# Performance work log

Measured on AMD Instinct MI355X. Metric: run time of the kernel, lower is better.

Reference implementation:

```python
import jax, jax.numpy as jnp
import numpy as np

B, P, H, W = 8, 128, 32, 32
NC = 4                 # num_classes = NUM_REL_GROUP + 1
DOBJ = 4424            # 2*DOBJ = 8848
CIN = 256
C = 128 + 8848         # 8976 GCN channel dim


def setup_inputs() -> dict:
    key = jax.random.key(0)
    ks = jax.random.split(key, 24)
    s = 0.02  # weight scale to keep activations moderate
    inp = {
        "x": jax.random.normal(ks[0], (B, CIN, H, W), jnp.float32),
        "rel_pair_idxs": jax.random.randint(ks[1], (B, P, 2), 0, 640, dtype=jnp.int32),
        "obj_rep": jax.random.normal(ks[2], (640, DOBJ), jnp.float32),
        # ADD_GCN params
        "fc_w": jax.random.normal(ks[3], (NC, CIN), jnp.float32) * s,
        "ct_w": jax.random.normal(ks[4], (128, CIN), jnp.float32) * s,
        "ct_b": jnp.zeros((128,), jnp.float32),
        # DynamicGraphConvolution params
        "A": jax.random.normal(ks[5], (NC, NC), jnp.float32) * 0.25,          # static_adj conv1d (no bias)
        "sw_w": jax.random.normal(ks[6], (C, C), jnp.float32) * s / np.sqrt(C) * 30,
        "sw_b": jnp.zeros((C,), jnp.float32),
        "cg_w": jax.random.normal(ks[7], (C, C), jnp.float32) * s / np.sqrt(C) * 30,
        "cg_b": jnp.zeros((C,), jnp.float32),
        "bn_g": jnp.ones((C,), jnp.float32),
        "bn_b": jnp.zeros((C,), jnp.float32),
        "bn_m": jnp.zeros((C,), jnp.float32),
        "bn_v": jnp.ones((C,), jnp.float32),
        "co_w": jax.random.normal(ks[8], (NC, 2 * C), jnp.float32) * s / np.sqrt(C) * 30,
        "co_b": jnp.zeros((NC,), jnp.float32),
        "dw_w": jax.random.normal(ks[9], (C, C), jnp.float32) * s / np.sqrt(C) * 30,
        "dw_b": jnp.zeros((C,), jnp.float32),
        "ll_w": jax.random.normal(ks[10], (NC, C), jnp.float32) * s / np.sqrt(C) * 30,
        "ll_b": jnp.zeros((NC,), jnp.float32),
        "mask_mat": jnp.eye(NC, dtype=jnp.float32),
    }
    return inp


def reference(x, rel_pair_idxs, obj_rep, fc_w, ct_w, ct_b, A, sw_w, sw_b,
              cg_w, cg_b, bn_g, bn_b, bn_m, bn_v, co_w, co_b, dw_w, dw_b,
              ll_w, ll_b, mask_mat):
    leaky = lambda t: jax.nn.leaky_relu(t, 0.2)
    b, cin, h, w = x.shape
    xr = x.reshape(b, cin, h * w)                                  # (B,256,HW)

    # forward_classification_sm: fc -> topk(1).mean == max over spatial
    y = jnp.einsum('oc,bcs->bos', fc_w, xr)                        # (B,NC,HW)
    out1 = y.max(-1)                                               # (B,NC)

    # forward_sam
    mask = jax.nn.sigmoid(y)                                       # (B,NC,HW)
    v = jnp.einsum('oc,bcs->bos', ct_w, xr) + ct_b[None, :, None]  # (B,128,HW)
    v = jnp.einsum('bcs,bns->bcn', v, mask)                        # (B,128,NC)

    # pairwise object features (gather), tiled over NC node slots
    o1 = obj_rep[rel_pair_idxs[..., 0]]                            # (B,P,DOBJ)
    o2 = obj_rep[rel_pair_idxs[..., 1]]
    pf = jnp.concatenate([o1, o2], -1)                             # (B,P,8848)
    p = pf.shape[1]
    pf = jnp.broadcast_to(pf[..., None], pf.shape + (NC,))         # (B,P,8848,NC)
    vb = jnp.broadcast_to(v[:, None], (b, p) + v.shape[1:])        # (B,P,128,NC)
    g = jnp.concatenate([pf, vb], 2).reshape(b * p, C, NC)         # (BP,C,NC)

    # --- DynamicGraphConvolution ---
    # static GCN: node-mix conv1d (no bias) + leaky, then channel 1x1 conv + leaky
    xs = leaky(jnp.einsum('nm,pcm->pcn', A, g))                    # (BP,C,NC)
    xs = leaky(jnp.einsum('oc,pcn->pon', sw_w, xs) + sw_b[None, :, None])
    hg = g + xs

    # dynamic adjacency
    glb = hg.mean(-1)                                              # (BP,C) gap
    glb = glb @ cg_w.T + cg_b                                      # conv_global (1x1)
    glb = (glb - bn_m) * jax.lax.rsqrt(bn_v + 1e-5) * bn_g + bn_b  # BN (eval)
    glb = leaky(glb)
    # conv_create_co_mat over cat([glb_expand, hg], ch) without materializing cat
    adj = jax.nn.sigmoid(
        jnp.einsum('oc,pc->po', co_w[:, :C], glb)[:, :, None]
        + jnp.einsum('oc,pcn->pon', co_w[:, C:], hg)
        + co_b[None, :, None])                                     # (BP,NC,NC)

    # dynamic GCN
    hd = leaky(jnp.einsum('pcn,pnm->pcm', hg, adj))
    z = leaky(jnp.einsum('oc,pcn->pon', dw_w, hd) + dw_b[None, :, None])  # (BP,C,NC)

    # head: last_linear + leaky, masked diagonal sum
    out2 = leaky(jnp.einsum('oc,pcn->pon', ll_w, z) + ll_b[None, :, None])  # (BP,NC,NC)
    out2 = (out2 * jax.lax.stop_gradient(mask_mat)).sum(-1)        # (BP,NC)

    o1b = jnp.broadcast_to(out1[:, None], (b, p, NC)).reshape(b * p, NC)
    return ((o1b + out2) * 0.5).reshape(b, p, NC)
```

## Files before the change

kernel.cpp:

```cpp
#include <hip/hip_runtime.h>
#include <stdint.h>

#define DEVI __device__ __forceinline__

typedef unsigned short u16;
typedef __bf16 bf16x8 __attribute__((ext_vector_type(8)));
typedef float f32x4 __attribute__((ext_vector_type(4)));
typedef u16 u16x8 __attribute__((ext_vector_type(8)));

DEVI u16 f2bf(float f){
  union { float f; unsigned u; } v; v.f = f;
  unsigned r = v.u + 0x7FFFu + ((v.u >> 16) & 1u);
  return (u16)(r >> 16);
}
DEVI float bf2f(u16 h){
  union { unsigned u; float f; } v; v.u = ((unsigned)h) << 16;
  return v.f;
}
DEVI float lky(float t){ return t > 0.f ? t : 0.2f * t; }

#define GLD16(gp, lp) __builtin_amdgcn_global_load_lds( \
    (const __attribute__((address_space(1))) void*)(gp), \
    (__attribute__((address_space(3))) void*)(lp), 16, 0, 0)


DEVI void stage_half(const u16* __restrict__ G, size_t grow0, int kcol, int Kp,
                     u16* lds, int t)
{
  #pragma unroll
  for (int j = 0; j < 2; ++j){
    const int off16 = j*512 + t;
    const int rl = off16 >> 3, sl = off16 & 7;
    const u16* gp = G + (grow0 + rl)*(size_t)Kp + kcol + ((sl ^ (rl & 7))*8);
    GLD16(gp, lds + off16*8);
  }
}

template<int RB, int RA>
DEVI void ph_reads(const u16* __restrict__ Ab, const u16* __restrict__ Bb,
                   bf16x8 (&afr)[4][2], bf16x8 (&bfr)[4][2],
                   int wr, int wc, int l4, int l15)
{
  if constexpr (RA >= 0){
    #pragma unroll
    for (int m = 0; m < 4; ++m){
      const int r = wr*128 + RA*64 + m*16 + l15;
      afr[m][0] = *(const bf16x8*)&Ab[r*64 + (((0+l4) ^ (r & 7))*8)];
      afr[m][1] = *(const bf16x8*)&Ab[r*64 + (((4+l4) ^ (r & 7))*8)];
    }
  }
  if constexpr (RB >= 0){
    #pragma unroll
    for (int nn = 0; nn < 2; ++nn){
      const int r = wc*64 + (RB+nn)*16 + l15;
      bfr[RB+nn][0] = *(const bf16x8*)&Bb[r*64 + (((0+l4) ^ (r & 7))*8)];
      bfr[RB+nn][1] = *(const bf16x8*)&Bb[r*64 + (((4+l4) ^ (r & 7))*8)];
    }
  }
}

template<int MH, int NH, int VM>
DEVI void ph_mfma(bf16x8 (&afr)[4][2], bf16x8 (&bfr)[4][2], f32x4 (&acc)[8][4])
{
  __builtin_amdgcn_s_barrier();
  __builtin_amdgcn_s_setprio(1);
  #pragma unroll
  for (int m = 0; m < 4; ++m)
    #pragma unroll
    for (int nn = 0; nn < 2; ++nn)
      #pragma unroll
      for (int ks = 0; ks < 2; ++ks)
        acc[MH*4+m][NH+nn] = __builtin_amdgcn_mfma_f32_16x16x32_bf16(
            afr[m][ks], bfr[NH+nn][ks], acc[MH*4+m][NH+nn], 0, 0, 0);
  __builtin_amdgcn_s_setprio(0);
  if constexpr (VM == 4){
    asm volatile("s_waitcnt vmcnt(4)" ::: "memory");
  }
  __builtin_amdgcn_s_barrier();
}

template<int EPI>
__global__ __launch_bounds__(512, 2)
void gemm256(const u16* __restrict__ A, const u16* __restrict__ B,
             int Kp, int Nt, int SN, int Mreal, float* __restrict__ C, long long ldc,
             const float* __restrict__ bias, const float* __restrict__ scale,
             const float* __restrict__ off, const float* __restrict__ llw,
             float* __restrict__ oacc,
             int ngemm, const float* __restrict__ cvt_src, int cvt_srows,
             int cvt_scols, int cvt_lstride, u16* __restrict__ cvt_dst,
             int cvt_kp, int cvt_prows, int cvt_nblk)
{
  __shared__ __align__(16) u16 As[2][16384];
  __shared__ __align__(16) u16 Bs[2][16384];

  if ((int)blockIdx.x >= ngemm){
    const int bid = blockIdx.x - ngemm;
    const int nch = cvt_kp >> 3;
    for (int r = bid; r < cvt_prows; r += cvt_nblk){
      for (int ch = threadIdx.x; ch < nch; ch += 512){
        const int k = ch*8;
        u16 o[8];
        if (r < cvt_srows){
          #pragma unroll
          for (int i=0;i<8;i++){
            const int kk = k + i;
            o[i] = (kk < cvt_scols) ? f2bf(cvt_src[(size_t)r*cvt_lstride + kk]) : (u16)0;
          }
        } else {
          #pragma unroll
          for (int i=0;i<8;i++) o[i] = 0;
        }
        u16x8 vv = { o[0],o[1],o[2],o[3],o[4],o[5],o[6],o[7] };
        *(u16x8*)&cvt_dst[(size_t)r*cvt_kp + k] = vv;
      }
    }
    return;
  }

  const int t    = threadIdx.x;
  const int lane = t & 63;
  const int wid  = t >> 6;
  const int wr = wid >> 2, wc = wid & 3;
  const int l4 = lane >> 4, l15 = lane & 15;

  const int nwg = ngemm;
  const int xc = blockIdx.x & 7, pp = blockIdx.x >> 3;
  const int qq = nwg >> 3, rr = nwg & 7;
  const int wg = (xc < rr ? xc*(qq+1) : rr*(qq+1) + (xc-rr)*qq) + pp;
  const int strip_sz = (nwg / Nt) * SN;
  const int strip = wg / strip_sz, srem = wg % strip_sz;
  const int mt = srem / SN, nt = strip*SN + srem % SN;

  const size_t am0 = (size_t)mt*256;
  const size_t bn0 = (size_t)nt*256;

  f32x4 acc[8][4];
  #pragma unroll
  for (int i = 0; i < 8; ++i)
    #pragma unroll
    for (int j = 0; j < 4; ++j) acc[i][j] = f32x4{0.f,0.f,0.f,0.f};
  bf16x8 afr[4][2], bfr[4][2];

  const int NT2 = Kp >> 6;
  const int NI  = NT2 >> 1;

  stage_half(A, am0+0,   0,  Kp, &As[0][0],    t);
  stage_half(A, am0+128, 0,  Kp, &As[0][8192], t);
  stage_half(B, bn0+0,   0,  Kp, &Bs[0][0],    t);
  stage_half(B, bn0+128, 0,  Kp, &Bs[0][8192], t);
  stage_half(B, bn0+0,   64, Kp, &Bs[1][0],    t);
  stage_half(B, bn0+128, 64, Kp, &Bs[1][8192], t);
  asm volatile("s_waitcnt vmcnt(4)" ::: "memory");
  __builtin_amdgcn_s_barrier();

  for (int i = 0; i < NI; ++i){
    const int k1  = 2*i + 1;
    const int ts0 = (2*i+2 < NT2) ? 2*i+2 : 2*i;
    const int ts1 = (2*i+3 < NT2) ? 2*i+3 : 2*i+1;
    ph_reads<0,0>(&As[0][0], &Bs[0][0], afr, bfr, wr, wc, l4, l15);
    stage_half(A, am0+0,   k1*64,  Kp, &As[1][0],    t);
    ph_mfma<0,0,-1>(afr, bfr, acc);
    ph_reads<2,-1>(&As[0][0], &Bs[0][0], afr, bfr, wr, wc, l4, l15);
    stage_half(A, am0+128, k1*64,  Kp, &As[1][8192], t);
    ph_mfma<0,2,-1>(afr, bfr, acc);
    ph_reads<-1,1>(&As[0][0], &Bs[0][0], afr, bfr, wr, wc, l4, l15);
    stage_half(B, bn0+0,   ts0*64, Kp, &Bs[0][0],    t);
    ph_mfma<1,2,-1>(afr, bfr, acc);
    stage_half(B, bn0+128, ts0*64, Kp, &Bs[0][8192], t);
    ph_mfma<1,0,4>(afr, bfr, acc);
    ph_reads<0,0>(&As[1][0], &Bs[1][0], afr, bfr, wr, wc, l4, l15);
    stage_half(A, am0+0,   ts0*64, Kp, &As[0][0],    t);
    ph_mfma<0,0,-1>(afr, bfr, acc);
    ph_reads<2,-1>(&As[1][0], &Bs[1][0], afr, bfr, wr, wc, l4, l15);
    stage_half(A, am0+128, ts0*64, Kp, &As[0][8192], t);
    ph_mfma<0,2,-1>(afr, bfr, acc);
    ph_reads<-1,1>(&As[1][0], &Bs[1][0], afr, bfr, wr, wc, l4, l15);
    stage_half(B, bn0+0,   ts1*64, Kp, &Bs[1][0],    t);
    ph_mfma<1,2,-1>(afr, bfr, acc);
    stage_half(B, bn0+128, ts1*64, Kp, &Bs[1][8192], t);
    ph_mfma<1,0,4>(afr, bfr, acc);
  }
  asm volatile("s_waitcnt vmcnt(0)" ::: "memory");

  const int ob0 = mt*256 + wr*128;
  const int nb0 = nt*256 + wc*64;

  if (EPI == 0){
    #pragma unroll
    for (int mi = 0; mi < 8; ++mi){
      const int ob = ob0 + mi*16 + l4*4;
      if (ob < Mreal){
        #pragma unroll
        for (int ni = 0; ni < 4; ++ni){
          const int n = nb0 + ni*16 + l15;
          *(f32x4*)&C[(size_t)n*ldc + ob] = acc[mi][ni];
        }
      }
    }
  } else if (EPI == 2){
    #pragma unroll
    for (int mi = 0; mi < 8; ++mi){
      const int ob = ob0 + mi*16 + l4*4;
      if (ob < Mreal){
        const float sc0=scale[ob],sc1=scale[ob+1],sc2=scale[ob+2],sc3=scale[ob+3];
        const float of0=off[ob],of1=off[ob+1],of2=off[ob+2],of3=off[ob+3];
        #pragma unroll
        for (int ni = 0; ni < 4; ++ni){
          const int n = nb0 + ni*16 + l15;
          f32x4 a = acc[mi][ni];
          f32x4 vv = { lky(a[0]*sc0+of0), lky(a[1]*sc1+of1),
                       lky(a[2]*sc2+of2), lky(a[3]*sc3+of3) };
          *(f32x4*)&C[(size_t)n*ldc + ob] = vv;
        }
      }
    }
  } else {
    #pragma unroll
    for (int ni = 0; ni < 4; ++ni){
      float s0=0.f, s1=0.f, s2=0.f, s3=0.f;
      #pragma unroll
      for (int mi = 0; mi < 8; ++mi){
        #pragma unroll
        for (int r = 0; r < 4; ++r){
          const int o = ob0 + mi*16 + l4*4 + r;
          if (o < Mreal){
            const float val = lky(acc[mi][ni][r] + bias[o]);
            s0 += llw[o]         * val;
            s1 += llw[8976 + o]  * val;
            s2 += llw[17952 + o] * val;
            s3 += llw[26928 + o] * val;
          }
        }
      }
      const int n = nb0 + ni*16 + l15;
      const int q = n >> 2, m = n & 3;
      float sv[4] = {s0,s1,s2,s3};
      #pragma unroll
      for (int o4 = 0; o4 < 4; ++o4){
        float tt = sv[o4];
        tt += __shfl_xor(tt, 16);
        tt += __shfl_xor(tt, 32);
        if (l4 == 0) atomicAdd(&oacc[(q*4 + o4)*4 + m], tt);
      }
    }
  }
}

__global__ __launch_bounds__(256)
void gemm_vpre(const u16* __restrict__ A, const u16* __restrict__ B,
               int Kp, int Nt, int Mreal, float* __restrict__ C, long long ldc,
               const float* __restrict__ bias)
{
  __shared__ __align__(16) u16 As[2][4096];
  __shared__ __align__(16) u16 Bs[2][4096];
  const int tid  = threadIdx.x;
  const int lane = tid & 63;
  const int wr   = (tid >> 6) >> 1, wc = (tid >> 6) & 1;
  const int l4   = lane >> 4, l15 = lane & 15;
  const int mt   = blockIdx.x / Nt, nt = blockIdx.x % Nt;

  const size_t arow = (size_t)(mt*128 + (tid>>2)) * Kp + (tid&3)*8;
  const size_t brow = (size_t)(nt*128 + (tid>>2)) * Kp + (tid&3)*8;
  const int    ldst = (tid>>2)*32 + (tid&3)*8;
  const size_t rowskip = (size_t)64 * Kp;

  f32x4 acc[4][4];
  #pragma unroll
  for (int i=0;i<4;i++)
    #pragma unroll
    for (int j=0;j<4;j++) acc[i][j] = f32x4{0.f,0.f,0.f,0.f};

  const int NT = Kp >> 5;
  {
    const u16* a0 = A + arow; const u16* b0 = B + brow;
    GLD16(a0,           &As[0][ldst]);
    GLD16(a0 + rowskip, &As[0][ldst + 2048]);
    GLD16(b0,           &Bs[0][ldst]);
    GLD16(b0 + rowskip, &Bs[0][ldst + 2048]);
  }
  __syncthreads();

  for (int kt=0; kt<NT; ++kt){
    const int cur = kt & 1;
    if (kt + 1 < NT){
      const u16* a0 = A + arow + (size_t)(kt+1)*32;
      const u16* b0 = B + brow + (size_t)(kt+1)*32;
      GLD16(a0,           &As[cur^1][ldst]);
      GLD16(a0 + rowskip, &As[cur^1][ldst + 2048]);
      GLD16(b0,           &Bs[cur^1][ldst]);
      GLD16(b0 + rowskip, &Bs[cur^1][ldst + 2048]);
    }
    bf16x8 af[4], bf[4];
    #pragma unroll
    for (int mi=0;mi<4;mi++)
      af[mi] = *(const bf16x8*)&As[cur][(wr*64 + mi*16 + l15)*32 + l4*8];
    #pragma unroll
    for (int ni=0;ni<4;ni++)
      bf[ni] = *(const bf16x8*)&Bs[cur][(wc*64 + ni*16 + l15)*32 + l4*8];
    #pragma unroll
    for (int mi=0;mi<4;mi++)
      #pragma unroll
      for (int ni=0;ni<4;ni++)
        acc[mi][ni] = __builtin_amdgcn_mfma_f32_16x16x32_bf16(af[mi], bf[ni], acc[mi][ni], 0, 0, 0);
    __syncthreads();
  }

  const int ob0 = mt*128 + wr*64;
  const int nb0 = nt*128 + wc*64;
  #pragma unroll
  for (int mi=0;mi<4;mi++)
    #pragma unroll
    for (int r=0;r<4;r++){
      const int o = ob0 + mi*16 + l4*4 + r;
      if (o < Mreal){
        const float bb = bias[o];
        #pragma unroll
        for (int ni=0;ni<4;ni++){
          const int n = nb0 + ni*16 + l15;
          C[(size_t)o*ldc + n] = acc[mi][ni][r] + bb;
        }
      }
    }
}

__global__ void k_cvt_pad(const float* __restrict__ src, int srows, int scols,
                          int lds_, int koff, u16* __restrict__ dst, int Kp)
{
  const int r = blockIdx.x;
  const int nch = Kp >> 3;
  for (int ch = threadIdx.x; ch < nch; ch += blockDim.x){
    const int k = ch*8;
    u16 o[8];
    if (r < srows){
      #pragma unroll
      for (int i=0;i<8;i++){
        const int kk = k + i;
        o[i] = (kk < scols) ? f2bf(src[(size_t)r*lds_ + koff + kk]) : (u16)0;
      }
    } else {
      #pragma unroll
      for (int i=0;i<8;i++) o[i] = 0;
    }
    u16x8 vv = { o[0],o[1],o[2],o[3],o[4],o[5],o[6],o[7] };
    *(u16x8*)&dst[(size_t)r*Kp + k] = vv;
  }
}

__global__ void k_cvt_obj(const float* __restrict__ obj, u16* __restrict__ dst)
{
  const int r = blockIdx.x;
  const int ab = (r >= 640);
  const float* src = obj + (size_t)(ab ? r-640 : r)*4424;
  for (int ch = threadIdx.x; ch < 560; ch += 256){
    const int k = ch*8;
    u16 o[8];
    #pragma unroll
    for (int i=0;i<8;i++){
      const int kk = k+i;
      float f = (kk < 4424) ? src[kk] : 0.f;
      if (ab) f = fabsf(f);
      o[i] = f2bf(f);
    }
    u16x8 vv = { o[0],o[1],o[2],o[3],o[4],o[5],o[6],o[7] };
    *(u16x8*)&dst[(size_t)r*4480 + k] = vv;
  }
}

__global__ void k_xT(const float* __restrict__ x, u16* __restrict__ xT)
{
  __shared__ float t[32][33];
  const int bid = blockIdx.x;
  const int b = bid >> 8; const int cs = (bid >> 5) & 7; const int ss = bid & 31;
  const int tx = threadIdx.x & 31, ty = threadIdx.x >> 5;
  #pragma unroll
  for (int i=0;i<4;i++){
    const int r = ty + i*8;
    t[r][tx] = x[((size_t)(b*256 + cs*32 + r))*1024 + ss*32 + tx];
  }
  __syncthreads();
  #pragma unroll
  for (int i=0;i<4;i++){
    const int r = ty + i*8;
    xT[((size_t)(b*1024 + ss*32 + r))*256 + cs*32 + tx] = f2bf(t[tx][r]);
  }
}

__global__ void k_ymask(const float* __restrict__ x, const float* __restrict__ fcw,
                        float* __restrict__ y, float* __restrict__ mask)
{
  __shared__ float fc[1024];
  const int b = blockIdx.x >> 2, st = blockIdx.x & 3;
  for (int i=threadIdx.x; i<1024; i+=256) fc[i] = fcw[i];
  __syncthreads();
  const int s = st*256 + threadIdx.x;
  float a0=0,a1=0,a2=0,a3=0;
  for (int c=0;c<256;c++){
    const float xv = x[((size_t)(b*256+c))*1024 + s];
    a0 += fc[c]*xv; a1 += fc[256+c]*xv; a2 += fc[512+c]*xv; a3 += fc[768+c]*xv;
  }
  const size_t base = (size_t)(b*4)*1024 + s;
  y[base]        = a0; mask[base]        = 1.f/(1.f+expf(-a0));
  y[base+1024]   = a1; mask[base+1024]   = 1.f/(1.f+expf(-a1));
  y[base+2048]   = a2; mask[base+2048]   = 1.f/(1.f+expf(-a2));
  y[base+3072]   = a3; mask[base+3072]   = 1.f/(1.f+expf(-a3));
}

__global__ void k_out1(const float* __restrict__ y, float* __restrict__ out1){
  const int bn = blockIdx.x;
  float m = -3.4e38f;
  for (int s=threadIdx.x; s<1024; s+=256) m = fmaxf(m, y[(size_t)bn*1024+s]);
  for (int o=32;o;o>>=1) m = fmaxf(m, __shfl_xor(m,o));
  __shared__ float red[4];
  if ((threadIdx.x&63)==0) red[threadIdx.x>>6] = m;
  __syncthreads();
  if (threadIdx.x==0) out1[bn] = fmaxf(fmaxf(red[0],red[1]),fmaxf(red[2],red[3]));
}

__global__ void k_v(const float* __restrict__ vpreT, const float* __restrict__ mask,
                    float* __restrict__ v){
  const int b = blockIdx.x >> 7, j = blockIdx.x & 127;
  float a[4]={0,0,0,0};
  for (int s=threadIdx.x; s<1024; s+=256){
    const float pv = vpreT[(size_t)j*8192 + b*1024 + s];
    #pragma unroll
    for (int m=0;m<4;m++) a[m] += pv * mask[((size_t)(b*4+m))*1024 + s];
  }
  __shared__ float red[4][5];
  #pragma unroll
  for (int m=0;m<4;m++){
    float t=a[m];
    for (int o=32;o;o>>=1) t += __shfl_xor(t,o);
    if ((threadIdx.x&63)==0) red[m][threadIdx.x>>6]=t;
  }
  __syncthreads();
  if (threadIdx.x<4)
    v[(size_t)(b*128+j)*4 + threadIdx.x] =
      red[threadIdx.x][0]+red[threadIdx.x][1]+red[threadIdx.x][2]+red[threadIdx.x][3];
}

__global__ void k_lv(const float* __restrict__ Am, const float* __restrict__ v,
                     float* __restrict__ lv){
  const int idx = blockIdx.x*256 + threadIdx.x;
  if (idx < 1024){
    #pragma unroll
    for (int n=0;n<4;n++){
      float s=0;
      #pragma unroll
      for (int m=0;m<4;m++) s += Am[n*4+m]*v[idx*4+m];
      lv[idx*4+n] = lky(s);
    }
  }
}

__global__ void k_sV(const float* __restrict__ sw, const float* __restrict__ lv,
                     float* __restrict__ sV){
  __shared__ float l[4096];
  for (int i=threadIdx.x; i<4096; i+=256) l[i]=lv[i];
  __syncthreads();
  const int o = blockIdx.x*256 + threadIdx.x;
  if (o >= 8976) return;
  float acc[8][4] = {};
  const float* row = sw + (size_t)o*8976 + 8848;
  for (int j=0;j<128;j++){
    const float wv = row[j];
    #pragma unroll
    for (int b=0;b<8;b++){
      const float* lb = &l[(b*128+j)*4];
      #pragma unroll
      for (int n=0;n<4;n++) acc[b][n] += wv*lb[n];
    }
  }
  #pragma unroll
  for (int b=0;b<8;b++){
    f32x4 vv = {acc[b][0],acc[b][1],acc[b][2],acc[b][3]};
    *(f32x4*)&sV[((size_t)b*8976 + o)*4] = vv;
  }
}

__global__ void k_so(const float* __restrict__ cgb, const float* __restrict__ g,
                     const float* __restrict__ b2, const float* __restrict__ m,
                     const float* __restrict__ vvar, float* __restrict__ so){
  const int o = blockIdx.x*256+threadIdx.x;
  if (o<8976){
    const float sc = g[o]*rsqrtf(vvar[o]+1e-5f);
    so[o]=sc; so[8976+o] = (cgb[o]-m[o])*sc + b2[o];
  }
}

__global__ void k_glb_t2(const float* __restrict__ U, const float* __restrict__ obj,
                         const int* __restrict__ rel,
                         const float* __restrict__ sV, const float* __restrict__ swb,
                         const float* __restrict__ v, const float* __restrict__ Am,
                         const float* __restrict__ cow, u16* __restrict__ glbB,
                         float* __restrict__ t2)
{
  const int q = blockIdx.x; const int b = q >> 7;
  const int i1 = rel[q*2], i2 = rel[q*2+1];
  const float* u1  = U + (size_t)i1*17952;
  const float* u2  = U + (size_t)i2*17952 + 8976;
  const float* u1a = U + (size_t)(640+i1)*17952;
  const float* u2a = U + (size_t)(640+i2)*17952 + 8976;
  const float* o1 = obj + (size_t)i1*4424;
  const float* o2 = obj + (size_t)i2*4424;
  float rA[4], aA[4];
  #pragma unroll
  for (int n=0;n<4;n++){
    const float s = Am[n*4]+Am[n*4+1]+Am[n*4+2]+Am[n*4+3];
    rA[n]=0.6f*s; aA[n]=0.4f*fabsf(s);
  }
  float t2a[16] = {};
  for (int c = threadIdx.x; c < 9088; c += 256){
    if (c < 8976){
      const float p1 = u1[c] + u2[c];
      const float p2 = u1a[c] + u2a[c];
      const f32x4 sv = *(const f32x4*)&sV[((size_t)b*8976 + c)*4];
      const float sb = swb[c];
      const float gs = (c < 4424) ? o1[c] : (c < 8848) ? o2[c-4424] : 0.f;
      float hg[4]; float sum = 0.f;
      #pragma unroll
      for (int n=0;n<4;n++){
        const float xs2 = lky(rA[n]*p1 + aA[n]*p2 + sv[n] + sb);
        const float g = (c < 8848) ? gs : v[((size_t)b*128 + (c-8848))*4 + n];
        hg[n] = g + xs2; sum += hg[n];
      }
      glbB[(size_t)q*9088 + c] = f2bf(0.25f*sum);
      #pragma unroll
      for (int o4=0;o4<4;o4++){
        const float cw = cow[(size_t)o4*17952 + 8976 + c];
        #pragma unroll
        for (int n=0;n<4;n++) t2a[o4*4+n] += cw*hg[n];
      }
    } else {
      glbB[(size_t)q*9088 + c] = 0;
    }
  }
  __shared__ float red[16][5];
  #pragma unroll
  for (int i=0;i<16;i++){
    float t = t2a[i];
    for (int o=32;o;o>>=1) t += __shfl_xor(t,o);
    if ((threadIdx.x&63)==0) red[i][threadIdx.x>>6]=t;
  }
  __syncthreads();
  if (threadIdx.x < 16)
    t2[q*16+threadIdx.x] = red[threadIdx.x][0]+red[threadIdx.x][1]
                          +red[threadIdx.x][2]+red[threadIdx.x][3];
}

__global__ void k_adj(const float* __restrict__ glb2, const float* __restrict__ cow,
                      const float* __restrict__ t2, const float* __restrict__ cob,
                      float* __restrict__ adj)
{
  const int q = blockIdx.x;
  float a[4]={0,0,0,0};
  for (int c=threadIdx.x; c<8976; c+=256){
    const float g = glb2[(size_t)q*8976+c];
    #pragma unroll
    for (int o=0;o<4;o++) a[o] += cow[(size_t)o*17952 + c]*g;
  }
  __shared__ float red[4][5]; __shared__ float co1[4];
  #pragma unroll
  for (int i=0;i<4;i++){
    float t=a[i]; for (int o=32;o;o>>=1) t += __shfl_xor(t,o);
    if ((threadIdx.x&63)==0) red[i][threadIdx.x>>6]=t;
  }
  __syncthreads();
  if (threadIdx.x<4)
    co1[threadIdx.x]=red[threadIdx.x][0]+red[threadIdx.x][1]+red[threadIdx.x][2]+red[threadIdx.x][3];
  __syncthreads();
  if (threadIdx.x<16){
    const int a_=threadIdx.x>>2, m=threadIdx.x&3;
    const float t = co1[a_] + t2[q*16 + a_*4 + m] + cob[a_];
    adj[q*16 + a_*4 + m] = 1.f/(1.f+expf(-t));
  }
}

__global__ void k_hd(const float* __restrict__ U, const float* __restrict__ obj,
                     const int* __restrict__ rel,
                     const float* __restrict__ sV, const float* __restrict__ swb,
                     const float* __restrict__ v, const float* __restrict__ Am,
                     const float* __restrict__ adj, u16* __restrict__ hdb)
{
  const int q = blockIdx.x; const int b = q>>7;
  const int i1 = rel[q*2], i2 = rel[q*2+1];
  const float* u1  = U + (size_t)i1*17952;
  const float* u2  = U + (size_t)i2*17952 + 8976;
  const float* u1a = U + (size_t)(640+i1)*17952;
  const float* u2a = U + (size_t)(640+i2)*17952 + 8976;
  const float* o1 = obj + (size_t)i1*4424;
  const float* o2 = obj + (size_t)i2*4424;
  float rA[4], aA[4];
  #pragma unroll
  for (int n=0;n<4;n++){
    const float s = Am[n*4]+Am[n*4+1]+Am[n*4+2]+Am[n*4+3];
    rA[n]=0.6f*s; aA[n]=0.4f*fabsf(s);
  }
  __shared__ float aj[16];
  if (threadIdx.x<16) aj[threadIdx.x] = adj[q*16+threadIdx.x];
  __syncthreads();
  float ajr[16];
  #pragma unroll
  for (int i=0;i<16;i++) ajr[i]=aj[i];
  for (int c=threadIdx.x; c<9088; c+=256){
    if (c<8976){
      const float p1 = u1[c] + u2[c];
      const float p2 = u1a[c] + u2a[c];
      const f32x4 sv = *(const f32x4*)&sV[((size_t)b*8976 + c)*4];
      const float sb = swb[c];
      const float gs = (c < 4424) ? o1[c] : (c < 8848) ? o2[c-4424] : 0.f;
      float hg[4];
      #pragma unroll
      for (int n=0;n<4;n++){
        const float xs2 = lky(rA[n]*p1 + aA[n]*p2 + sv[n] + sb);
        const float g = (c < 8848) ? gs : v[((size_t)b*128 + (c-8848))*4 + n];
        hg[n] = g + xs2;
      }
      #pragma unroll
      for (int m=0;m<4;m++){
        const float hv = lky(hg[0]*ajr[m] + hg[1]*ajr[4+m] + hg[2]*ajr[8+m] + hg[3]*ajr[12+m]);
        hdb[((size_t)(q*4+m))*9088 + c] = f2bf(hv);
      }
    } else {
      #pragma unroll
      for (int m=0;m<4;m++) hdb[((size_t)(q*4+m))*9088 + c] = 0;
    }
  }
}

__global__ void k_final(const float* __restrict__ o2f, const float* __restrict__ out1,
                        const float* __restrict__ llb, const float* __restrict__ mm,
                        float* __restrict__ out)
{
  const int idx = blockIdx.x*256+threadIdx.x;
  if (idx < 4096){
    const int q = idx>>2, o = idx&3, b = q>>7;
    float s=0.f;
    #pragma unroll
    for (int m=0;m<4;m++) s += lky(o2f[(q*4+o)*4+m] + llb[o]) * mm[o*4+m];
    out[idx] = 0.5f*(out1[b*4+o] + s);
  }
}

extern "C" void kernel_launch(void* const* d_in, const int* in_sizes, int n_in,
                              void* d_out, int out_size, void* d_ws, size_t ws_size,
                              hipStream_t stream)
{
  const float* x    = (const float*)d_in[0];
  const int*   rel  = (const int*)d_in[1];
  const float* obj  = (const float*)d_in[2];
  const float* fcw  = (const float*)d_in[3];
  const float* ctw  = (const float*)d_in[4];
  const float* ctb  = (const float*)d_in[5];
  const float* Am   = (const float*)d_in[6];
  const float* sww  = (const float*)d_in[7];
  const float* swb  = (const float*)d_in[8];
  const float* cgw  = (const float*)d_in[9];
  const float* cgb  = (const float*)d_in[10];
  const float* bng  = (const float*)d_in[11];
  const float* bnb  = (const float*)d_in[12];
  const float* bnm  = (const float*)d_in[13];
  const float* bnv  = (const float*)d_in[14];
  const float* cow  = (const float*)d_in[15];
  const float* cob  = (const float*)d_in[16];
  const float* dww  = (const float*)d_in[17];
  const float* dwb  = (const float*)d_in[18];
  const float* llw  = (const float*)d_in[19];
  const float* llb  = (const float*)d_in[20];
  const float* mm   = (const float*)d_in[21];
  float* out = (float*)d_out;
  (void)in_sizes; (void)n_in; (void)out_size;

  const size_t WB = (size_t)9216*9088*2;
  char* ws = (char*)d_ws;
  size_t off = 0;
  auto alloc = [&](size_t bytes)->char*{
    char* p = ws + off; off = (off + bytes + 255) & ~(size_t)255; return p;
  };

  const size_t SMALL = (size_t)91914240 + 18612224 + 74448896 + 11468800
                     + 36765696 + 4194304 + 65536 + 131072 + 131072 + 256
                     + 4194304 + 16384 + 16384 + 1148928 + 71808 + 65536*3
                     + 64*1024;
  const bool fused = (ws_size >= 2*WB + SMALL);

  u16* WbA = (u16*)alloc(WB);
  u16* WbB = fused ? (u16*)alloc(WB) : WbA;
  float* U     = (float*)alloc((size_t)1280*17952*4);
  u16*   glbB  = (u16*)  alloc((size_t)1024*9088*2);
  u16*   hdb   = (u16*)  alloc((size_t)4096*9088*2);
  u16*   objB  = (u16*)  alloc((size_t)1280*4480*2);
  float* glb2  = (float*)alloc((size_t)1024*8976*4);
  u16*   xT    = (u16*)  alloc((size_t)8192*256*2);
  u16*   ctwb  = (u16*)  alloc((size_t)128*256*2);
  float* y     = (float*)alloc((size_t)32768*4);
  float* mask  = (float*)alloc((size_t)32768*4);
  float* out1  = (float*)alloc((size_t)32*4);
  float* vpreT = (float*)alloc((size_t)128*8192*4);
  float* v     = (float*)alloc((size_t)4096*4);
  float* lv    = (float*)alloc((size_t)4096*4);
  float* sV    = (float*)alloc((size_t)287232*4);
  float* so    = (float*)alloc((size_t)2*8976*4);
  float* t2    = (float*)alloc((size_t)16384*4);
  float* adj   = (float*)alloc((size_t)16384*4);
  float* o2f   = (float*)alloc((size_t)16384*4);

  k_xT<<<dim3(2048), dim3(256), 0, stream>>>(x, xT);
  k_cvt_pad<<<dim3(128), dim3(256), 0, stream>>>(ctw, 128, 256, 256, 0, ctwb, 256);
  k_ymask<<<dim3(32), dim3(256), 0, stream>>>(x, fcw, y, mask);
  k_out1<<<dim3(32), dim3(256), 0, stream>>>(y, out1);
  gemm_vpre<<<dim3(64), dim3(256), 0, stream>>>(
      ctwb, xT, 256, 64, 128, vpreT, (long long)8192, ctb);
  k_v<<<dim3(1024), dim3(256), 0, stream>>>(vpreT, mask, v);

  k_cvt_obj<<<dim3(1280), dim3(256), 0, stream>>>(obj, objB);
  k_cvt_pad<<<dim3(8976), dim3(256), 0, stream>>>(sww, 8976, 4424, 8976, 0, WbA, 4480);
  k_cvt_pad<<<dim3(9200), dim3(256), 0, stream>>>(sww, 8976, 4424, 8976, 4424,
                                                  WbA + (size_t)8976*4480, 4480);
  if (fused){
    gemm256<0><<<dim3(512), dim3(512), 0, stream>>>(
        WbA, objB, 4480, 5, 5, 17952, U, (long long)17952,
        nullptr, nullptr, nullptr, nullptr, nullptr,
        355, cgw, 8976, 8976, 8976, WbB, 9088, 9216, 157);
  } else {
    gemm256<0><<<dim3(355), dim3(512), 0, stream>>>(
        WbA, objB, 4480, 5, 5, 17952, U, (long long)17952,
        nullptr, nullptr, nullptr, nullptr, nullptr,
        355, nullptr, 0, 0, 0, nullptr, 8, 0, 1);
  }

  k_lv<<<dim3(4), dim3(256), 0, stream>>>(Am, v, lv);
  k_sV<<<dim3(36), dim3(256), 0, stream>>>(sww, lv, sV);
  k_glb_t2<<<dim3(1024), dim3(256), 0, stream>>>(U, obj, rel, sV, swb, v, Am,
                                                 cow, glbB, t2);

  if (!fused)
    k_cvt_pad<<<dim3(9216), dim3(256), 0, stream>>>(cgw, 8976, 8976, 8976, 0, WbB, 9088);
  k_so<<<dim3(36), dim3(256), 0, stream>>>(cgb, bng, bnb, bnm, bnv, so);
  if (fused){
    gemm256<2><<<dim3(256), dim3(512), 0, stream>>>(
        WbB, glbB, 9088, 4, 4, 8976, glb2, (long long)8976,
        nullptr, so, so + 8976, nullptr, nullptr,
        144, dww, 8976, 8976, 8976, WbA, 9088, 9216, 112);
  } else {
    gemm256<2><<<dim3(144), dim3(512), 0, stream>>>(
        WbB, glbB, 9088, 4, 4, 8976, glb2, (long long)8976,
        nullptr, so, so + 8976, nullptr, nullptr,
        144, nullptr, 0, 0, 0, nullptr, 8, 0, 1);
  }

  k_adj<<<dim3(1024), dim3(256), 0, stream>>>(glb2, cow, t2, cob, adj);
  if (!fused)
    k_cvt_pad<<<dim3(9216), dim3(256), 0, stream>>>(dww, 8976, 8976, 8976, 0, WbA, 9088);
  k_hd<<<dim3(1024), dim3(256), 0, stream>>>(U, obj, rel, sV, swb, v, Am, adj, hdb);

  hipMemsetAsync(o2f, 0, (size_t)16384*4, stream);
  gemm256<3><<<dim3(576), dim3(512), 0, stream>>>(
      WbA, hdb, 9088, 16, 8, 8976, nullptr, 0, dwb,
      nullptr, nullptr, llw, o2f,
      576, nullptr, 0, 0, 0, nullptr, 8, 0, 1);

  k_final<<<dim3(16), dim3(256), 0, stream>>>(o2f, out1, llb, mm, out);
}
```

Measured before the change: 2.142 ms.

## Add 128x256-tile triple-buffered GEMM for U and final dynamic-weight GEMMs

Adds a new gemm128 kernel with a 128-row by 256-column tile, a three-stage LDS ring buffer and an XCD-aware workgroup remap. It replaces the 256x256 kernel for the first GEMM (sw_w times obj) and for the final dw_w GEMM with the fused last-linear epilogue. To make the K dimension divisible by 64*3, the K padding becomes 4608 and 9216. The conversion of cg_w into the weight buffer is no longer fused into the first GEMM and always runs as a separate kernel. The smaller tiles give more workgroups and better tail balance, at the cost of lower data reuse per tile and extra padded K work.

Result: slower. 2.241 ms (+4.6%).

```diff
diff --git a/kernel.cpp b/kernel.cpp
--- a/kernel.cpp
+++ b/kernel.cpp
@@ -23,6 +23,157 @@
     (const __attribute__((address_space(1))) void*)(gp), \
     (__attribute__((address_space(3))) void*)(lp), 16, 0, 0)
 
+template<int J>
+DEVI void stageN(const u16* __restrict__ G, size_t grow0, int kcol, int Kp,
+                 u16* lds, int t)
+{
+  #pragma unroll
+  for (int j = 0; j < J; ++j){
+    const int off16 = j*512 + t;
+    const int rl = off16 >> 3, sl = off16 & 7;
+    const u16* gp = G + (grow0 + rl)*(size_t)Kp + kcol + ((sl ^ (rl & 7))*8);
+    GLD16(gp, lds + off16*8);
+  }
+}
+
+template<int VM>
+DEVI void mf16(bf16x8 (&afr)[4], bf16x8 (&bfr)[4], f32x4 (&acc)[4][4])
+{
+  __builtin_amdgcn_s_barrier();
+  __builtin_amdgcn_s_setprio(1);
+  #pragma unroll
+  for (int m = 0; m < 4; ++m)
+    #pragma unroll
+    for (int n = 0; n < 4; ++n)
+      acc[m][n] = __builtin_amdgcn_mfma_f32_16x16x32_bf16(
+          afr[m], bfr[n], acc[m][n], 0, 0, 0);
+  __builtin_amdgcn_s_setprio(0);
+  if constexpr (VM == 6){
+    asm volatile("s_waitcnt vmcnt(6)" ::: "memory");
+  }
+  __builtin_amdgcn_s_barrier();
+}
+
+template<int EPI>
+__global__ __launch_bounds__(512, 2)
+void gemm128(const u16* __restrict__ A, const u16* __restrict__ B,
+             int Kp, int Nt, int Mreal, float* __restrict__ C, long long ldc,
+             const float* __restrict__ bias, const float* __restrict__ llw,
+             float* __restrict__ oacc)
+{
+  __shared__ __align__(16) u16 As[3][8192];
+  __shared__ __align__(16) u16 Bs[3][16384];
+  const int t    = threadIdx.x;
+  const int lane = t & 63;
+  const int wid  = t >> 6;
+  const int wr = wid >> 2, wc = wid & 3;
+  const int l4 = lane >> 4, l15 = lane & 15;
+
+  const int nwg = gridDim.x;
+  const int xc = blockIdx.x & 7, pp = blockIdx.x >> 3;
+  const int qq = nwg >> 3, rr = nwg & 7;
+  const int wg = (xc < rr ? xc*(qq+1) : rr*(qq+1) + (xc-rr)*qq) + pp;
+  const int mt = wg / Nt, nt = wg % Nt;
+
+  const size_t am0 = (size_t)mt*128;
+  const size_t bn0 = (size_t)nt*256;
+
+  f32x4 acc[4][4];
+  #pragma unroll
+  for (int i = 0; i < 4; ++i)
+    #pragma unroll
+    for (int j = 0; j < 4; ++j) acc[i][j] = f32x4{0.f,0.f,0.f,0.f};
+  bf16x8 afr[4], bfr[4];
+
+  const int NT2 = Kp >> 6;
+  const int NG  = NT2 / 3;
+
+  auto RD = [&](const u16* __restrict__ Ab, const u16* __restrict__ Bb, int ks){
+    #pragma unroll
+    for (int m = 0; m < 4; ++m){
+      const int r = wr*64 + m*16 + l15;
+      afr[m] = *(const bf16x8*)&Ab[r*64 + (((ks*4 + l4) ^ (r & 7))*8)];
+    }
+    #pragma unroll
+    for (int n = 0; n < 4; ++n){
+      const int r = wc*64 + n*16 + l15;
+      bfr[n] = *(const bf16x8*)&Bb[r*64 + (((ks*4 + l4) ^ (r & 7))*8)];
+    }
+  };
+
+  stageN<2>(A, am0, 0,  Kp, &As[0][0], t);
+  stageN<4>(B, bn0, 0,  Kp, &Bs[0][0], t);
+  stageN<2>(A, am0, 64, Kp, &As[1][0], t);
+  stageN<4>(B, bn0, 64, Kp, &Bs[1][0], t);
+  asm volatile("s_waitcnt vmcnt(6)" ::: "memory");
+  __builtin_amdgcn_s_barrier();
+
+  for (int g = 0; g < NG; ++g){
+    const int t0 = 3*g;
+    const int p2 = (t0+2 < NT2) ? t0+2 : NT2-1;
+    const int p3 = (t0+3 < NT2) ? t0+3 : NT2-1;
+    const int p4 = (t0+4 < NT2) ? t0+4 : NT2-1;
+    RD(&As[0][0], &Bs[0][0], 0); stageN<2>(A, am0, p2*64, Kp, &As[2][0], t);
+    mf16<-1>(afr, bfr, acc);
+    RD(&As[0][0], &Bs[0][0], 1); stageN<4>(B, bn0, p2*64, Kp, &Bs[2][0], t);
+    mf16<6>(afr, bfr, acc);
+    RD(&As[1][0], &Bs[1][0], 0); stageN<2>(A, am0, p3*64, Kp, &As[0][0], t);
+    mf16<-1>(afr, bfr, acc);
+    RD(&As[1][0], &Bs[1][0], 1); stageN<4>(B, bn0, p3*64, Kp, &Bs[0][0], t);
+    mf16<6>(afr, bfr, acc);
+    RD(&As[2][0], &Bs[2][0], 0); stageN<2>(A, am0, p4*64, Kp, &As[1][0], t);
+    mf16<-1>(afr, bfr, acc);
+    RD(&As[2][0], &Bs[2][0], 1); stageN<4>(B, bn0, p4*64, Kp, &Bs[1][0], t);
+    mf16<6>(afr, bfr, acc);
+  }
+  asm volatile("s_waitcnt vmcnt(0)" ::: "memory");
+
+  const int ob0 = mt*128 + wr*64;
+  const int nb0 = nt*256 + wc*64;
+
+  if (EPI == 0){
+    #pragma unroll
+    for (int mi = 0; mi < 4; ++mi){
+      const int ob = ob0 + mi*16 + l4*4;
+      if (ob < Mreal){
+        #pragma unroll
+        for (int ni = 0; ni < 4; ++ni){
+          const int n = nb0 + ni*16 + l15;
+          *(f32x4*)&C[(size_t)n*ldc + ob] = acc[mi][ni];
+        }
+      }
+    }
+  } else {
+    #pragma unroll
+    for (int ni = 0; ni < 4; ++ni){
+      float s0=0.f, s1=0.f, s2=0.f, s3=0.f;
+      #pragma unroll
+      for (int mi = 0; mi < 4; ++mi){
+        #pragma unroll
+        for (int r = 0; r < 4; ++r){
+          const int o = ob0 + mi*16 + l4*4 + r;
+          if (o < Mreal){
+            const float val = lky(acc[mi][ni][r] + bias[o]);
+            s0 += llw[o]         * val;
+            s1 += llw[8976 + o]  * val;
+            s2 += llw[17952 + o] * val;
+            s3 += llw[26928 + o] * val;
+          }
+        }
+      }
+      const int n = nb0 + ni*16 + l15;
+      const int q = n >> 2, m = n & 3;
+      float sv[4] = {s0,s1,s2,s3};
+      #pragma unroll
+      for (int o4 = 0; o4 < 4; ++o4){
+        float tt = sv[o4];
+        tt += __shfl_xor(tt, 16);
+        tt += __shfl_xor(tt, 32);
+        if (l4 == 0) atomicAdd(&oacc[(q*4 + o4)*4 + m], tt);
+      }
+    }
+  }
+}
 
 DEVI void stage_half(const u16* __restrict__ G, size_t grow0, int kcol, int Kp,
                      u16* lds, int t)
@@ -79,13 +230,10 @@
   __builtin_amdgcn_s_barrier();
 }
 
-template<int EPI>
 __global__ __launch_bounds__(512, 2)
 void gemm256(const u16* __restrict__ A, const u16* __restrict__ B,
              int Kp, int Nt, int SN, int Mreal, float* __restrict__ C, long long ldc,
-             const float* __restrict__ bias, const float* __restrict__ scale,
-             const float* __restrict__ off, const float* __restrict__ llw,
-             float* __restrict__ oacc,
+             const float* __restrict__ scale, const float* __restrict__ off,
              int ngemm, const float* __restrict__ cvt_src, int cvt_srows,
              int cvt_scols, int cvt_lstride, u16* __restrict__ cvt_dst,
              int cvt_kp, int cvt_prows, int cvt_nblk)
@@ -184,63 +332,19 @@
 
   const int ob0 = mt*256 + wr*128;
   const int nb0 = nt*256 + wc*64;
-
-  if (EPI == 0){
-    #pragma unroll
-    for (int mi = 0; mi < 8; ++mi){
-      const int ob = ob0 + mi*16 + l4*4;
-      if (ob < Mreal){
-        #pragma unroll
-        for (int ni = 0; ni < 4; ++ni){
-          const int n = nb0 + ni*16 + l15;
-          *(f32x4*)&C[(size_t)n*ldc + ob] = acc[mi][ni];
-        }
-      }
-    }
-  } else if (EPI == 2){
-    #pragma unroll
-    for (int mi = 0; mi < 8; ++mi){
-      const int ob = ob0 + mi*16 + l4*4;
-      if (ob < Mreal){
-        const float sc0=scale[ob],sc1=scale[ob+1],sc2=scale[ob+2],sc3=scale[ob+3];
-        const float of0=off[ob],of1=off[ob+1],of2=off[ob+2],of3=off[ob+3];
-        #pragma unroll
-        for (int ni = 0; ni < 4; ++ni){
-          const int n = nb0 + ni*16 + l15;
-          f32x4 a = acc[mi][ni];
-          f32x4 vv = { lky(a[0]*sc0+of0), lky(a[1]*sc1+of1),
-                       lky(a[2]*sc2+of2), lky(a[3]*sc3+of3) };
-          *(f32x4*)&C[(size_t)n*ldc + ob] = vv;
-        }
-      }
-    }
-  } else {
-    #pragma unroll
-    for (int ni = 0; ni < 4; ++ni){
-      float s0=0.f, s1=0.f, s2=0.f, s3=0.f;
-      #pragma unroll
-      for (int mi = 0; mi < 8; ++mi){
-        #pragma unroll
-        for (int r = 0; r < 4; ++r){
-          const int o = ob0 + mi*16 + l4*4 + r;
-          if (o < Mreal){
-            const float val = lky(acc[mi][ni][r] + bias[o]);
-            s0 += llw[o]         * val;
-            s1 += llw[8976 + o]  * val;
-            s2 += llw[17952 + o] * val;
-            s3 += llw[26928 + o] * val;
-          }
-        }
-      }
-      const int n = nb0 + ni*16 + l15;
-      const int q = n >> 2, m = n & 3;
-      float sv[4] = {s0,s1,s2,s3};
-      #pragma unroll
-      for (int o4 = 0; o4 < 4; ++o4){
-        float tt = sv[o4];
-        tt += __shfl_xor(tt, 16);
-        tt += __shfl_xor(tt, 32);
-        if (l4 == 0) atomicAdd(&oacc[(q*4 + o4)*4 + m], tt);
+  #pragma unroll
+  for (int mi = 0; mi < 8; ++mi){
+    const int ob = ob0 + mi*16 + l4*4;
+    if (ob < Mreal){
+      const float sc0=scale[ob],sc1=scale[ob+1],sc2=scale[ob+2],sc3=scale[ob+3];
+      const float of0=off[ob],of1=off[ob+1],of2=off[ob+2],of3=off[ob+3];
+      #pragma unroll
+      for (int ni = 0; ni < 4; ++ni){
+        const int n = nb0 + ni*16 + l15;
+        f32x4 a = acc[mi][ni];
+        f32x4 vv = { lky(a[0]*sc0+of0), lky(a[1]*sc1+of1),
+                     lky(a[2]*sc2+of2), lky(a[3]*sc3+of3) };
+        *(f32x4*)&C[(size_t)n*ldc + ob] = vv;
       }
     }
   }
@@ -351,7 +455,7 @@
   const int r = blockIdx.x;
   const int ab = (r >= 640);
   const float* src = obj + (size_t)(ab ? r-640 : r)*4424;
-  for (int ch = threadIdx.x; ch < 560; ch += 256){
+  for (int ch = threadIdx.x; ch < 576; ch += 256){
     const int k = ch*8;
     u16 o[8];
     #pragma unroll
@@ -362,7 +466,7 @@
       o[i] = f2bf(f);
     }
     u16x8 vv = { o[0],o[1],o[2],o[3],o[4],o[5],o[6],o[7] };
-    *(u16x8*)&dst[(size_t)r*4480 + k] = vv;
+    *(u16x8*)&dst[(size_t)r*4608 + k] = vv;
   }
 }
 
@@ -509,7 +613,7 @@
     rA[n]=0.6f*s; aA[n]=0.4f*fabsf(s);
   }
   float t2a[16] = {};
-  for (int c = threadIdx.x; c < 9088; c += 256){
+  for (int c = threadIdx.x; c < 9216; c += 256){
     if (c < 8976){
       const float p1 = u1[c] + u2[c];
       const float p2 = u1a[c] + u2a[c];
@@ -523,7 +627,7 @@
         const float g = (c < 8848) ? gs : v[((size_t)b*128 + (c-8848))*4 + n];
         hg[n] = g + xs2; sum += hg[n];
       }
-      glbB[(size_t)q*9088 + c] = f2bf(0.25f*sum);
+      glbB[(size_t)q*9216 + c] = f2bf(0.25f*sum);
       #pragma unroll
       for (int o4=0;o4<4;o4++){
         const float cw = cow[(size_t)o4*17952 + 8976 + c];
@@ -531,7 +635,7 @@
         for (int n=0;n<4;n++) t2a[o4*4+n] += cw*hg[n];
       }
     } else {
-      glbB[(size_t)q*9088 + c] = 0;
+      glbB[(size_t)q*9216 + c] = 0;
     }
   }
   __shared__ float red[16][5];
@@ -601,7 +705,7 @@
   float ajr[16];
   #pragma unroll
   for (int i=0;i<16;i++) ajr[i]=aj[i];
-  for (int c=threadIdx.x; c<9088; c+=256){
+  for (int c=threadIdx.x; c<9216; c+=256){
     if (c<8976){
       const float p1 = u1[c] + u2[c];
       const float p2 = u1a[c] + u2a[c];
@@ -618,11 +722,11 @@
       #pragma unroll
       for (int m=0;m<4;m++){
         const float hv = lky(hg[0]*ajr[m] + hg[1]*ajr[4+m] + hg[2]*ajr[8+m] + hg[3]*ajr[12+m]);
-        hdb[((size_t)(q*4+m))*9088 + c] = f2bf(hv);
+        hdb[((size_t)(q*4+m))*9216 + c] = f2bf(hv);
       }
     } else {
       #pragma unroll
-      for (int m=0;m<4;m++) hdb[((size_t)(q*4+m))*9088 + c] = 0;
+      for (int m=0;m<4;m++) hdb[((size_t)(q*4+m))*9216 + c] = 0;
     }
   }
 }
@@ -670,25 +774,22 @@
   float* out = (float*)d_out;
   (void)in_sizes; (void)n_in; (void)out_size;
 
-  const size_t WB = (size_t)9216*9088*2;
+  const size_t WB = (size_t)9216*9216*2;
   char* ws = (char*)d_ws;
   size_t off = 0;
   auto alloc = [&](size_t bytes)->char*{
     char* p = ws + off; off = (off + bytes + 255) & ~(size_t)255; return p;
   };
 
-  const size_t SMALL = (size_t)91914240 + 18612224 + 74448896 + 11468800
-                     + 36765696 + 4194304 + 65536 + 131072 + 131072 + 256
-                     + 4194304 + 16384 + 16384 + 1148928 + 71808 + 65536*3
-                     + 64*1024;
-  const bool fused = (ws_size >= 2*WB + SMALL);
+  const size_t SMALL = (size_t)250*1024*1024;
+  const bool two_buf = (ws_size >= 2*WB + SMALL);
 
   u16* WbA = (u16*)alloc(WB);
-  u16* WbB = fused ? (u16*)alloc(WB) : WbA;
+  u16* WbB = two_buf ? (u16*)alloc(WB) : WbA;
   float* U     = (float*)alloc((size_t)1280*17952*4);
-  u16*   glbB  = (u16*)  alloc((size_t)1024*9088*2);
-  u16*   hdb   = (u16*)  alloc((size_t)4096*9088*2);
-  u16*   objB  = (u16*)  alloc((size_t)1280*4480*2);
+  u16*   glbB  = (u16*)  alloc((size_t)1024*9216*2);
+  u16*   hdb   = (u16*)  alloc((size_t)4096*9216*2);
+  u16*   objB  = (u16*)  alloc((size_t)1280*4608*2);
   float* glb2  = (float*)alloc((size_t)1024*8976*4);
   u16*   xT    = (u16*)  alloc((size_t)8192*256*2);
   u16*   ctwb  = (u16*)  alloc((size_t)128*256*2);
@@ -713,51 +814,37 @@
   k_v<<<dim3(1024), dim3(256), 0, stream>>>(vpreT, mask, v);
 
   k_cvt_obj<<<dim3(1280), dim3(256), 0, stream>>>(obj, objB);
-  k_cvt_pad<<<dim3(8976), dim3(256), 0, stream>>>(sww, 8976, 4424, 8976, 0, WbA, 4480);
+  k_cvt_pad<<<dim3(8976), dim3(256), 0, stream>>>(sww, 8976, 4424, 8976, 0, WbA, 4608);
   k_cvt_pad<<<dim3(9200), dim3(256), 0, stream>>>(sww, 8976, 4424, 8976, 4424,
-                                                  WbA + (size_t)8976*4480, 4480);
-  if (fused){
-    gemm256<0><<<dim3(512), dim3(512), 0, stream>>>(
-        WbA, objB, 4480, 5, 5, 17952, U, (long long)17952,
-        nullptr, nullptr, nullptr, nullptr, nullptr,
-        355, cgw, 8976, 8976, 8976, WbB, 9088, 9216, 157);
-  } else {
-    gemm256<0><<<dim3(355), dim3(512), 0, stream>>>(
-        WbA, objB, 4480, 5, 5, 17952, U, (long long)17952,
-        nullptr, nullptr, nullptr, nullptr, nullptr,
-        355, nullptr, 0, 0, 0, nullptr, 8, 0, 1);
-  }
+                                                  WbA + (size_t)8976*4608, 4608);
+  gemm128<0><<<dim3(141*5), dim3(512), 0, stream>>>(
+      WbA, objB, 4608, 5, 17952, U, (long long)17952, nullptr, nullptr, nullptr);
 
   k_lv<<<dim3(4), dim3(256), 0, stream>>>(Am, v, lv);
   k_sV<<<dim3(36), dim3(256), 0, stream>>>(sww, lv, sV);
   k_glb_t2<<<dim3(1024), dim3(256), 0, stream>>>(U, obj, rel, sV, swb, v, Am,
                                                  cow, glbB, t2);
 
-  if (!fused)
-    k_cvt_pad<<<dim3(9216), dim3(256), 0, stream>>>(cgw, 8976, 8976, 8976, 0, WbB, 9088);
+  k_cvt_pad<<<dim3(9216), dim3(256), 0, stream>>>(cgw, 8976, 8976, 8976, 0, WbB, 9216);
   k_so<<<dim3(36), dim3(256), 0, stream>>>(cgb, bng, bnb, bnm, bnv, so);
-  if (fused){
-    gemm256<2><<<dim3(256), dim3(512), 0, stream>>>(
-        WbB, glbB, 9088, 4, 4, 8976, glb2, (long long)8976,
-        nullptr, so, so + 8976, nullptr, nullptr,
-        144, dww, 8976, 8976, 8976, WbA, 9088, 9216, 112);
+  if (two_buf){
+    gemm256<<<dim3(256), dim3(512), 0, stream>>>(
+        WbB, glbB, 9216, 4, 4, 8976, glb2, (long long)8976, so, so + 8976,
+        144, dww, 8976, 8976, 8976, WbA, 9216, 9216, 112);
   } else {
-    gemm256<2><<<dim3(144), dim3(512), 0, stream>>>(
-        WbB, glbB, 9088, 4, 4, 8976, glb2, (long long)8976,
-        nullptr, so, so + 8976, nullptr, nullptr,
+    gemm256<<<dim3(144), dim3(512), 0, stream>>>(
+        WbB, glbB, 9216, 4, 4, 8976, glb2, (long long)8976, so, so + 8976,
         144, nullptr, 0, 0, 0, nullptr, 8, 0, 1);
   }
 
   k_adj<<<dim3(1024), dim3(256), 0, stream>>>(glb2, cow, t2, cob, adj);
-  if (!fused)
-    k_cvt_pad<<<dim3(9216), dim3(256), 0, stream>>>(dww, 8976, 8976, 8976, 0, WbA, 9088);
+  if (!two_buf)
+    k_cvt_pad<<<dim3(9216), dim3(256), 0, stream>>>(dww, 8976, 8976, 8976, 0, WbA, 9216);
   k_hd<<<dim3(1024), dim3(256), 0, stream>>>(U, obj, rel, sV, swb, v, Am, adj, hdb);
 
   hipMemsetAsync(o2f, 0, (size_t)16384*4, stream);
-  gemm256<3><<<dim3(576), dim3(512), 0, stream>>>(
-      WbA, hdb, 9088, 16, 8, 8976, nullptr, 0, dwb,
-      nullptr, nullptr, llw, o2f,
-      576, nullptr, 0, 0, 0, nullptr, 8, 0, 1);
+  gemm128<3><<<dim3(71*16), dim3(512), 0, stream>>>(
+      WbA, hdb, 9216, 16, 8976, nullptr, 0, dwb, llw, o2f);
 
   k_final<<<dim3(16), dim3(256), 0, stream>>>(o2f, out1, llb, mm, out);
 }
```
